# Kernel optimization log

Measured on AMD Instinct MI355X. Metric: run time of the kernel, lower is better.

## Reference

```python
import jax, jax.numpy as jnp
import numpy as np

B, T, S, H = 8, 512, 512, 768
VOCAB = 32110  # hardcoded in the original module


def setup_inputs() -> dict:
    key = jax.random.key(0)
    k1, k2, k3, k4, k5 = jax.random.split(key, 5)
    return {
        "decoder_input_embeds": jax.random.normal(k1, (B, T, H), dtype=jnp.float32),
        "sequence_output": jax.random.normal(k2, (B, T, H), dtype=jnp.float32),
        "cross_attentions": jax.random.uniform(k3, (B, T, S), dtype=jnp.float32),
        "input_ids_to_copy": jax.random.randint(k4, (B, S), 0, VOCAB, dtype=jnp.int64),
        "w_pgen": jax.random.normal(k5, (2 * H, 1), dtype=jnp.float32) * 0.02,
        "b_pgen": jnp.zeros((1,), dtype=jnp.float32),
    }


def reference(decoder_input_embeds, sequence_output, cross_attentions,
              input_ids_to_copy, w_pgen, b_pgen):
    # p_gen = sigmoid(Linear(concat(dec_embeds, seq_out)))  -> [B, T, 1]
    total_states = jnp.concatenate((decoder_input_embeds, sequence_output), axis=-1)
    p_gen = jax.nn.sigmoid(total_states @ w_pgen + b_pgen)

    # logits[b, t, v] = sum_{s : ids[b,s]==v} attn[b, t, s]
    # (math-equivalent to attn @ one_hot(ids), done as a scatter-add)
    def per_batch(attn_bts, ids_s):  # attn [T, S], ids [S]
        return jax.ops.segment_sum(attn_bts.T, ids_s, num_segments=VOCAB).T  # [T, V]

    logits = jax.vmap(per_batch)(cross_attentions, input_ids_to_copy)  # [B, T, V]
    return p_gen, logits
```

## Files before the change

kernel.cpp:

```cpp
#include <hip/hip_runtime.h>
#include <math.h>

#define BB 8
#define TT 512
#define SS 512
#define HH 768
#define VOCAB 32110
#define QCHUNK 8028
#define NROWS (BB * TT)
#define LDSF (QCHUNK + 4)

__global__ __launch_bounds__(256) void pgen_kernel(
    const float* __restrict__ dec,
    const float* __restrict__ seq,
    const float* __restrict__ w,
    const float* __restrict__ bptr,
    float* __restrict__ out)
{
    const int gid  = blockIdx.x * 256 + threadIdx.x;
    const int row  = gid >> 6;
    const int lane = threadIdx.x & 63;
    if (row >= NROWS) return;

    const float* d = dec + (size_t)row * HH;
    const float* s = seq + (size_t)row * HH;

    float acc = 0.f;
    #pragma unroll
    for (int j0 = 0; j0 < HH; j0 += 256) {
        int j = j0 + lane * 4;
        float4 dv = *reinterpret_cast<const float4*>(d + j);
        float4 wv = *reinterpret_cast<const float4*>(w + j);
        float4 sv = *reinterpret_cast<const float4*>(s + j);
        float4 uv = *reinterpret_cast<const float4*>(w + HH + j);
        acc += dv.x * wv.x + dv.y * wv.y + dv.z * wv.z + dv.w * wv.w;
        acc += sv.x * uv.x + sv.y * uv.y + sv.z * uv.z + sv.w * uv.w;
    }
    #pragma unroll
    for (int off = 32; off > 0; off >>= 1)
        acc += __shfl_down(acc, off, 64);

    if (lane == 0) {
        float x = acc + bptr[0];
        out[row] = 1.f / (1.f + expf(-x));
    }
}

__global__ __launch_bounds__(512, 8) void scatter_logits(
    const float* __restrict__ attn,
    const int*   __restrict__ ids,
    float* __restrict__ out_logits)
{
    __shared__ float smem[LDSF];

    const int bid = blockIdx.x;
    const int q   = bid >> 12;
    const int row = bid & (NROWS - 1);
    const int b   = row >> 9;
    const int tid = threadIdx.x;

    const int lo    = q * QCHUNK;
    const int n     = (q == 3) ? (VOCAB - 3 * QCHUNK) : QCHUNK;
    const int shift = (row & 1) ? 2 : 0;

    float4* sm4 = reinterpret_cast<float4*>(smem);
    #pragma unroll
    for (int i = tid; i < LDSF / 4; i += 512) sm4[i] = make_float4(0.f, 0.f, 0.f, 0.f);
    __syncthreads();

    {
        const float* arow = attn + (size_t)row * SS;
        const int*   irow = ids  + (size_t)b * SS;
        int   v = irow[tid];
        float a = arow[tid];
        int loc = v - lo;
        if ((unsigned)loc < (unsigned)n) atomicAdd(&smem[loc + shift], a);
    }
    __syncthreads();

    float* dst = out_logits + (size_t)row * VOCAB + lo;

    if (shift && tid == 0) {
        *reinterpret_cast<float2*>(dst) = make_float2(smem[2], smem[3]);
    }
    const int main4 = (n - shift) >> 2;
    const int tail  = n - shift - 4 * main4;

    const float4* s4 = reinterpret_cast<const float4*>(smem + 2 * shift);
    float4*       d4 = reinterpret_cast<float4*>(dst + shift);
    #pragma unroll 2
    for (int i = tid; i < main4; i += 512) d4[i] = s4[i];

    if (tail && tid == 1) {
        *reinterpret_cast<float2*>(dst + shift + 4 * main4) =
            *reinterpret_cast<const float2*>(smem + 2 * shift + 4 * main4);
    }
}

extern "C" void kernel_launch(void* const* d_in, const int* in_sizes, int n_in,
                              void* d_out, int out_size, void* d_ws, size_t ws_size,
                              hipStream_t stream) {
    const float* dec  = (const float*)d_in[0];
    const float* seq  = (const float*)d_in[1];
    const float* attn = (const float*)d_in[2];
    const int*   ids  = (const int*)  d_in[3];
    const float* w    = (const float*)d_in[4];
    const float* bp   = (const float*)d_in[5];

    float* out = (float*)d_out;

    pgen_kernel<<<NROWS / 4, 256, 0, stream>>>(dec, seq, w, bp, out);
    scatter_logits<<<4 * NROWS, 512, 0, stream>>>(attn, ids, out + NROWS);
}
```

Before: 550.5 us.

## Process several rows per block with double-buffered LDS chunks

Each scatter block now handles 4 consecutive rows and loops over 8 smaller vocab chunks. Two LDS buffers alternate, and plain s_barrier with only an LDS waitcnt is used, so the global stores from one chunk can still be in flight while the next chunk is zeroed and scattered. The ids and attention values are loaded once per row instead of once per chunk block, and the grid shrinks from 16384 to 1024 blocks. The cost is less block-level parallelism, and correctness now depends on the hand-placed barriers and waitcnts.

Measured after the change: 550.2 us. About the same (-0.1%).

```diff
diff --git a/kernel.cpp b/kernel.cpp
--- a/kernel.cpp
+++ b/kernel.cpp
@@ -6,9 +6,13 @@
 #define SS 512
 #define HH 768
 #define VOCAB 32110
-#define QCHUNK 8028
 #define NROWS (BB * TT)
-#define LDSF (QCHUNK + 4)
+#define NCHUNK 4016
+#define NCH 8
+#define LASTN (VOCAB - 7 * NCHUNK)
+#define LDSPAD (NCHUNK + 4)
+#define ROWS_PER_BLK 4
+#define NBLK (NROWS / ROWS_PER_BLK)
 
 __global__ __launch_bounds__(256) void pgen_kernel(
     const float* __restrict__ dec,
@@ -51,49 +55,53 @@
     const int*   __restrict__ ids,
     float* __restrict__ out_logits)
 {
-    __shared__ float smem[LDSF];
+    __shared__ float smem[2][LDSPAD];
+    const int tid  = threadIdx.x;
+    const int row0 = blockIdx.x * ROWS_PER_BLK;
 
-    const int bid = blockIdx.x;
-    const int q   = bid >> 12;
-    const int row = bid & (NROWS - 1);
-    const int b   = row >> 9;
-    const int tid = threadIdx.x;
+    for (int r = 0; r < ROWS_PER_BLK; ++r) {
+        const int row = row0 + r;
+        const int b   = row >> 9;
+        const int v   = ids[b * SS + tid];
+        const float a = attn[(size_t)row * SS + tid];
+        const int shift = (row & 1) ? 2 : 0;
+        float* dstrow = out_logits + (size_t)row * VOCAB;
 
-    const int lo    = q * QCHUNK;
-    const int n     = (q == 3) ? (VOCAB - 3 * QCHUNK) : QCHUNK;
-    const int shift = (row & 1) ? 2 : 0;
+        for (int c = 0; c < NCH; ++c) {
+            float* sm = smem[c & 1];
+            const int lo = c * NCHUNK;
+            const int n  = (c == NCH - 1) ? LASTN : NCHUNK;
 
-    float4* sm4 = reinterpret_cast<float4*>(smem);
-    #pragma unroll
-    for (int i = tid; i < LDSF / 4; i += 512) sm4[i] = make_float4(0.f, 0.f, 0.f, 0.f);
-    __syncthreads();
+            float4* sm4 = reinterpret_cast<float4*>(sm);
+            sm4[tid] = make_float4(0.f, 0.f, 0.f, 0.f);
+            if (tid < (LDSPAD / 4) - 512)
+                sm4[tid + 512] = make_float4(0.f, 0.f, 0.f, 0.f);
 
-    {
-        const float* arow = attn + (size_t)row * SS;
-        const int*   irow = ids  + (size_t)b * SS;
-        int   v = irow[tid];
-        float a = arow[tid];
-        int loc = v - lo;
-        if ((unsigned)loc < (unsigned)n) atomicAdd(&smem[loc + shift], a);
-    }
-    __syncthreads();
+            asm volatile("s_waitcnt lgkmcnt(0)" ::: "memory");
+            __builtin_amdgcn_s_barrier();
 
-    float* dst = out_logits + (size_t)row * VOCAB + lo;
+            int loc = v - lo;
+            if ((unsigned)loc < (unsigned)n) atomicAdd(&sm[loc + shift], a);
 
-    if (shift && tid == 0) {
-        *reinterpret_cast<float2*>(dst) = make_float2(smem[2], smem[3]);
-    }
-    const int main4 = (n - shift) >> 2;
-    const int tail  = n - shift - 4 * main4;
+            asm volatile("s_waitcnt lgkmcnt(0)" ::: "memory");
+            __builtin_amdgcn_s_barrier();
 
-    const float4* s4 = reinterpret_cast<const float4*>(smem + 2 * shift);
-    float4*       d4 = reinterpret_cast<float4*>(dst + shift);
-    #pragma unroll 2
-    for (int i = tid; i < main4; i += 512) d4[i] = s4[i];
+            float* dst = dstrow + lo;
+            if (shift && tid == 0)
+                *reinterpret_cast<float2*>(dst) = make_float2(sm[2], sm[3]);
 
-    if (tail && tid == 1) {
-        *reinterpret_cast<float2*>(dst + shift + 4 * main4) =
-            *reinterpret_cast<const float2*>(smem + 2 * shift + 4 * main4);
+            const int main4 = (n - shift) >> 2;
+            const int tail  = n - shift - 4 * main4;
+
+            const float4* s4 = reinterpret_cast<const float4*>(sm + 2 * shift);
+            float4*       d4 = reinterpret_cast<float4*>(dst + shift);
+            #pragma unroll 2
+            for (int i = tid; i < main4; i += 512) d4[i] = s4[i];
+
+            if (tail && tid == 1)
+                *reinterpret_cast<float2*>(dst + shift + 4 * main4) =
+                    *reinterpret_cast<const float2*>(sm + 2 * shift + 4 * main4);
+        }
     }
 }
 
@@ -110,5 +118,5 @@
     float* out = (float*)d_out;
 
     pgen_kernel<<<NROWS / 4, 256, 0, stream>>>(dec, seq, w, bp, out);
-    scatter_logits<<<4 * NROWS, 512, 0, stream>>>(attn, ids, out + NROWS);
+    scatter_logits<<<NBLK, 512, 0, stream>>>(attn, ids, out + NROWS);
 }
```
